# Performance work log

Measured on AMD Instinct MI355X. Metric: run time of the kernel, lower is better.

Reference implementation:

```python
import jax, jax.numpy as jnp
import numpy as np

N_MEMORY = 128
INPUT_LEN = 512
OUTPUT_LEN = 256
N_FRAMES = 65536


def setup_inputs() -> dict:
    key = jax.random.key(0)
    k1, k2, k3, k4, k5 = jax.random.split(key, 5)
    return {
        "inputs": jax.random.normal(k1, (INPUT_LEN, N_FRAMES), dtype=jnp.float32),
        "W1": jax.random.normal(k2, (2 * N_MEMORY, INPUT_LEN), dtype=jnp.float32) * 0.05,
        "B1": jax.random.normal(k3, (2 * N_MEMORY, 1), dtype=jnp.float32) * 0.05,
        "W2": jax.random.normal(k4, (OUTPUT_LEN, N_MEMORY), dtype=jnp.float32) * 0.05,
        "B2": jax.random.normal(k5, (OUTPUT_LEN, 1), dtype=jnp.float32) * 0.05,
    }


def reference(inputs, W1, B1, W2, B2):
    # h: (2M, T)
    h = jax.nn.sigmoid(jnp.matmul(W1, inputs) + B1)
    M = W1.shape[0] // 2
    left, right = h[:M], h[M:]          # each (M, T)
    prod = left * right                  # gate product, (M, T)

    # Linear recurrence: u_0 = 0; u_t = prod[:, t-1] * u_{t-1} + (1 - left[:, t-1])
    # Affine pairs for t = 1..T-1, time-major: (T-1, M)
    a = prod[:, :-1].T
    b = (1.0 - left[:, :-1]).T

    def combine(c1, c2):
        a1, b1 = c1
        a2, b2 = c2
        return a1 * a2, a2 * b1 + b2

    _, bb = jax.lax.associative_scan(combine, (a, b))
    # u_0 = 0 => u_t = bb_t; prepend the zero initial state as column 0
    z = jnp.concatenate([jnp.zeros((M, 1), dtype=inputs.dtype), bb.T], axis=1)  # (M, T)

    out = 1.0 - jax.nn.sigmoid(jnp.matmul(W2, z) + B2)  # (output_len, T)
    return out
```

## Files before the change

kernel.cpp:

```cpp
#include <hip/hip_runtime.h>

typedef unsigned short u16;
typedef short bf16x8 __attribute__((ext_vector_type(8)));
typedef float f32x4 __attribute__((ext_vector_type(4)));

#define NF 65536
#define GCH 512

__device__ __forceinline__ float sigm(float x){ return 1.0f/(1.0f+__expf(-x)); }

__device__ __forceinline__ u16 f2bf(float f){
  union { float f; unsigned u; } v; v.f = f;
  unsigned r = (v.u + 0x7fffu + ((v.u >> 16) & 1u)) >> 16;
  return (u16)r;
}

#define AS1(p) ((const __attribute__((address_space(1))) unsigned int*)(p))
#define AS3(p) ((__attribute__((address_space(3))) unsigned int*)(p))

__global__ __launch_bounds__(256) void k_prep(const float* __restrict__ W1, const float* __restrict__ W2,
                                              u16* __restrict__ W1f, u16* __restrict__ W2f){
  int idx = blockIdx.x*256 + threadIdx.x;
  {
    int j  = idx & 7;
    int L  = (idx >> 3) & 63;
    int ks = (idx >> 9) & 1;
    int rt = (idx >> 10) & 15;
    int ck = idx >> 14;
    int row = 16*rt + (L & 15);
    int k   = ck*64 + ks*32 + ((L >> 4) << 3) + j;
    W1f[idx] = f2bf(W1[row*512 + k]);
  }
  if (idx < 32768){
    int j  = idx & 7;
    int L  = (idx >> 3) & 63;
    int ks = (idx >> 9) & 3;
    int rt = idx >> 11;
    int row = 16*rt + (L & 15);
    int m   = ks*32 + ((L >> 4) << 3) + j;
    W2f[idx] = f2bf(W2[row*128 + m]);
  }
}

__global__ __launch_bounds__(256) void k_tr(const float* __restrict__ x, u16* __restrict__ xT){
  __shared__ float ls[64*65];
  const int tid = threadIdx.x;
  const int bt = blockIdx.x & 1023, bk = blockIdx.x >> 10;
  const int T0 = bt*64, K0 = bk*64;
  #pragma unroll
  for (int l=0;l<4;l++){
    int idx = tid + l*256;
    int kl = idx >> 4, c4 = idx & 15;
    float4 v = *(const float4*)(x + (size_t)(K0+kl)*NF + T0 + c4*4);
    float* d = ls + kl*65 + c4*4;
    d[0]=v.x; d[1]=v.y; d[2]=v.z; d[3]=v.w;
  }
  __syncthreads();
  #pragma unroll
  for (int l=0;l<2;l++){
    int p = tid + l*256;
    int t = p >> 3, kb = p & 7;
    unsigned u[8];
    #pragma unroll
    for (int m=0;m<8;m++) u[m] = f2bf(ls[(kb*8+m)*65 + t]);
    uint4 pk;
    pk.x = u[0] | (u[1]<<16); pk.y = u[2] | (u[3]<<16);
    pk.z = u[4] | (u[5]<<16); pk.w = u[6] | (u[7]<<16);
    *(uint4*)(xT + (size_t)(T0+t)*512 + K0 + kb*8) = pk;
  }
}

__global__ __launch_bounds__(256, 2) void k_gemm1(const u16* __restrict__ xT,
        const u16* __restrict__ W1f, const float* __restrict__ B1,
        float* __restrict__ Aa, float* __restrict__ Bb,
        float* __restrict__ Ac, float* __restrict__ Bc){
  __shared__ __align__(16) u16 ws[16384];
  __shared__ __align__(16) u16 xs[8192];
  const int tid = threadIdx.x;
  const int wv = tid >> 6, L = tid & 63;
  const int q = L >> 4, ln = L & 15;
  const int g = blockIdx.x;
  const int F0 = g * 128;
  const int rt0 = 2*wv;

  f32x4 acc[4][8];
  #pragma unroll
  for (int a=0;a<4;a++)
    #pragma unroll
    for (int c=0;c<8;c++) acc[a][c] = (f32x4){0.f,0.f,0.f,0.f};

  for (int ck=0; ck<8; ++ck){
    #pragma unroll
    for (int i=0;i<8;i++){
      int s = wv*8 + i;
      __builtin_amdgcn_global_load_lds(AS1(W1f + ck*16384 + s*512 + L*8), AS3(ws + s*512), 16, 0, 0);
    }
    #pragma unroll
    for (int i=0;i<4;i++){
      int s = wv*4 + i;
      int c = s >> 1, ks = s & 1;
      int t = F0 + c*16 + ln;
      int k = ck*64 + ks*32 + q*8;
      __builtin_amdgcn_global_load_lds(AS1(xT + (size_t)t*512 + k), AS3(xs + s*512), 16, 0, 0);
    }
    __syncthreads();
    #pragma unroll
    for (int ks=0; ks<2; ++ks){
      bf16x8 af[4];
      af[0] = ((const bf16x8*)ws)[( rt0   *2+ks)*64 + L];
      af[1] = ((const bf16x8*)ws)[((rt0+1)*2+ks)*64 + L];
      af[2] = ((const bf16x8*)ws)[((rt0+8)*2+ks)*64 + L];
      af[3] = ((const bf16x8*)ws)[((rt0+9)*2+ks)*64 + L];
      #pragma unroll
      for (int c=0;c<8;c++){
        bf16x8 bf = ((const bf16x8*)xs)[(c*2+ks)*64 + L];
        acc[0][c] = __builtin_amdgcn_mfma_f32_16x16x32_bf16(af[0], bf, acc[0][c], 0,0,0);
        acc[1][c] = __builtin_amdgcn_mfma_f32_16x16x32_bf16(af[1], bf, acc[1][c], 0,0,0);
        acc[2][c] = __builtin_amdgcn_mfma_f32_16x16x32_bf16(af[2], bf, acc[2][c], 0,0,0);
        acc[3][c] = __builtin_amdgcn_mfma_f32_16x16x32_bf16(af[3], bf, acc[3][c], 0,0,0);
      }
    }
    __syncthreads();
  }
  #pragma unroll
  for (int pr=0; pr<2; ++pr){
    int mb = 32*wv + 16*pr + 4*q;
    float bl[4], br[4];
    #pragma unroll
    for (int r=0;r<4;r++){ bl[r] = B1[mb+r]; br[r] = B1[mb+128+r]; }
    float RA[4], RB[4];
    #pragma unroll
    for (int c=0;c<8;c++){
      int t = F0 + 16*c + ln;
      f32x4 Lv = acc[pr][c], Rv = acc[pr+2][c];
      float a4[4], b4[4];
      #pragma unroll
      for (int r=0;r<4;r++){
        float le = sigm(Lv[r] + bl[r]);
        float ri = sigm(Rv[r] + br[r]);
        a4[r] = le*ri; b4[r] = 1.0f - le;
      }
      *(float4*)(Aa + (size_t)t*128 + mb) = make_float4(a4[0],a4[1],a4[2],a4[3]);
      *(float4*)(Bb + (size_t)t*128 + mb) = make_float4(b4[0],b4[1],b4[2],b4[3]);
      #pragma unroll
      for (int r=0;r<4;r++){
        float As = a4[r], Bs = b4[r];
        #pragma unroll
        for (int d=1; d<16; d<<=1){
          float Ap = __shfl_xor(As, d);
          float Bp = __shfl_xor(Bs, d);
          Bs = (ln & d) ? fmaf(As, Bp, Bs) : fmaf(Ap, Bs, Bp);
          As *= Ap;
        }
        if (c == 0){ RA[r] = As; RB[r] = Bs; }
        else       { RB[r] = fmaf(As, RB[r], Bs); RA[r] *= As; }
      }
    }
    if (ln == 0){
      #pragma unroll
      for (int r=0;r<4;r++){
        Ac[g*128 + mb + r] = RA[r];
        Bc[g*128 + mb + r] = RB[r];
      }
    }
  }
}

__global__ __launch_bounds__(1024) void k_scan(const float* __restrict__ Ac, const float* __restrict__ Bc,
                                               float* __restrict__ Pb){
  __shared__ float sA[8][128], sB[8][128];
  const int tid = threadIdx.x;
  const int m = tid & 127, s = tid >> 7;
  const int g0 = s*64;
  float A = 1.f, B = 0.f;
  #pragma unroll 16
  for (int i=0;i<64;i++){
    float a = Ac[(g0+i)*128 + m], b = Bc[(g0+i)*128 + m];
    B = fmaf(a, B, b);
    A *= a;
  }
  sA[s][m] = A; sB[s][m] = B;
  __syncthreads();
  float v = 0.f;
  for (int s2=0; s2<s; ++s2) v = fmaf(sA[s2][m], v, sB[s2][m]);
  #pragma unroll 16
  for (int i=0;i<64;i++){
    int g = g0+i;
    Pb[g*128+m] = v;
    v = fmaf(Ac[g*128+m], v, Bc[g*128+m]);
  }
}

__global__ __launch_bounds__(512, 2) void k_apply(const float* __restrict__ Aa, const float* __restrict__ Bb,
        const float* __restrict__ Pb, const u16* __restrict__ W2f, const float* __restrict__ B2,
        float* __restrict__ out){
  __shared__ __align__(16) u16 zf[16384];
  __shared__ float sA[4][128], sB[4][128];
  const int tid = threadIdx.x;
  const int g = blockIdx.x, T0 = g*128;

  {
    const int m = tid & 127, s4 = tid >> 7;
    const float* ap = Aa + (size_t)(T0 + s4*32)*128 + m;
    const float* bp = Bb + (size_t)(T0 + s4*32)*128 + m;
    float areg[32], breg[32];
    #pragma unroll
    for (int i=0;i<32;i++){ areg[i] = ap[(size_t)i*128]; breg[i] = bp[(size_t)i*128]; }
    float A = 1.f, Bv = 0.f;
    #pragma unroll
    for (int i=0;i<32;i++){ Bv = fmaf(areg[i], Bv, breg[i]); A *= areg[i]; }
    sA[s4][m] = A; sB[s4][m] = Bv;
    __syncthreads();
    float v = Pb[g*128 + m];
    for (int s2=0; s2<s4; ++s2) v = fmaf(sA[s2][m], v, sB[s2][m]);
    const int base_m = (m>>5)*512 + ((m>>3)&3)*128 + (m&7);
    #pragma unroll
    for (int i=0;i<32;i++){
      int t = s4*32 + i;
      zf[base_m + (t>>4)*2048 + (t&15)*8] = f2bf(v);
      v = fmaf(areg[i], v, breg[i]);
    }
  }
  __syncthreads();

  const int wv = tid >> 6, L = tid & 63;
  const int q = L >> 4, ln = L & 15;
  f32x4 acc[2][8];
  #pragma unroll
  for (int a=0;a<2;a++)
    #pragma unroll
    for (int c=0;c<8;c++) acc[a][c] = (f32x4){0.f,0.f,0.f,0.f};

  #pragma unroll
  for (int ks=0; ks<4; ++ks){
    bf16x8 af0 = ((const bf16x8*)W2f)[((2*wv  )*4+ks)*64 + L];
    bf16x8 af1 = ((const bf16x8*)W2f)[((2*wv+1)*4+ks)*64 + L];
    #pragma unroll
    for (int c=0;c<8;c++){
      bf16x8 bf = ((const bf16x8*)zf)[(c*4+ks)*64 + L];
      acc[0][c] = __builtin_amdgcn_mfma_f32_16x16x32_bf16(af0, bf, acc[0][c], 0,0,0);
      acc[1][c] = __builtin_amdgcn_mfma_f32_16x16x32_bf16(af1, bf, acc[1][c], 0,0,0);
    }
  }

  #pragma unroll
  for (int rs=0;rs<2;rs++){
    int rowb = (2*wv+rs)*16 + q*4;
    float b2[4];
    #pragma unroll
    for (int r=0;r<4;r++) b2[r] = B2[rowb+r];
    #pragma unroll
    for (int c=0;c<8;c++){
      int t = T0 + 16*c + ln;
      #pragma unroll
      for (int r=0;r<4;r++)
        out[(size_t)(rowb+r)*NF + t] = sigm(-(acc[rs][c][r] + b2[r]));
    }
  }
}

extern "C" void kernel_launch(void* const* d_in, const int* in_sizes, int n_in,
                              void* d_out, int out_size, void* d_ws, size_t ws_size,
                              hipStream_t stream) {
  const float* x  = (const float*)d_in[0];
  const float* W1 = (const float*)d_in[1];
  const float* B1 = (const float*)d_in[2];
  const float* W2 = (const float*)d_in[3];
  const float* B2 = (const float*)d_in[4];
  float* out = (float*)d_out;

  u16*   W1f = (u16*)d_ws;
  u16*   W2f = W1f + 131072;
  float* Aa  = (float*)d_ws + 81920;
  float* Bb  = Aa + (size_t)NF*128;
  float* Ac  = Bb + (size_t)NF*128;
  float* Bc  = Ac + (size_t)GCH*128;
  float* Pb  = Bc + (size_t)GCH*128;
  u16*   xT  = (u16*)d_out;

  k_prep <<<512, 256, 0, stream>>>(W1, W2, W1f, W2f);
  k_tr   <<<8192, 256, 0, stream>>>(x, xT);
  k_gemm1<<<512, 256, 0, stream>>>(xT, W1f, B1, Aa, Bb, Ac, Bc);
  k_scan <<<1, 1024, 0, stream>>>(Ac, Bc, Pb);
  k_apply<<<GCH, 512, 0, stream>>>(Aa, Bb, Pb, W2f, B2, out);
}
```

Measured before the change: 338.3 us.

## Fuse input transpose into GEMM1 and fold chunk scan into apply kernel

Removes the separate transpose kernel: GEMM1 now loads fp32 input tiles directly into LDS, converts them to bf16 and re-lays them out in shared memory before the MFMAs. W1 fragments are read straight from global memory into registers instead of being staged through LDS. The single-block carry-scan kernel is removed; each apply block recomputes its own prefix over preceding chunk summaries with four thread groups. This cuts two launches and a full bf16 round trip of the input through global memory, at the cost of in-kernel conversion work, redundant prefix computation per block, and a loop without the old trailing barrier.

```diff
diff --git a/kernel.cpp b/kernel.cpp
--- a/kernel.cpp
+++ b/kernel.cpp
@@ -42,46 +42,19 @@
   }
 }
 
-__global__ __launch_bounds__(256) void k_tr(const float* __restrict__ x, u16* __restrict__ xT){
-  __shared__ float ls[64*65];
-  const int tid = threadIdx.x;
-  const int bt = blockIdx.x & 1023, bk = blockIdx.x >> 10;
-  const int T0 = bt*64, K0 = bk*64;
-  #pragma unroll
-  for (int l=0;l<4;l++){
-    int idx = tid + l*256;
-    int kl = idx >> 4, c4 = idx & 15;
-    float4 v = *(const float4*)(x + (size_t)(K0+kl)*NF + T0 + c4*4);
-    float* d = ls + kl*65 + c4*4;
-    d[0]=v.x; d[1]=v.y; d[2]=v.z; d[3]=v.w;
-  }
-  __syncthreads();
-  #pragma unroll
-  for (int l=0;l<2;l++){
-    int p = tid + l*256;
-    int t = p >> 3, kb = p & 7;
-    unsigned u[8];
-    #pragma unroll
-    for (int m=0;m<8;m++) u[m] = f2bf(ls[(kb*8+m)*65 + t]);
-    uint4 pk;
-    pk.x = u[0] | (u[1]<<16); pk.y = u[2] | (u[3]<<16);
-    pk.z = u[4] | (u[5]<<16); pk.w = u[6] | (u[7]<<16);
-    *(uint4*)(xT + (size_t)(T0+t)*512 + K0 + kb*8) = pk;
-  }
-}
-
-__global__ __launch_bounds__(256, 2) void k_gemm1(const u16* __restrict__ xT,
+__global__ __launch_bounds__(256, 2) void k_gemm1(const float* __restrict__ x,
         const u16* __restrict__ W1f, const float* __restrict__ B1,
         float* __restrict__ Aa, float* __restrict__ Bb,
         float* __restrict__ Ac, float* __restrict__ Bc){
-  __shared__ __align__(16) u16 ws[16384];
-  __shared__ __align__(16) u16 xs[8192];
+  __shared__ __align__(16) float ls[8192];
+  __shared__ __align__(16) u16  xs[8192];
   const int tid = threadIdx.x;
   const int wv = tid >> 6, L = tid & 63;
   const int q = L >> 4, ln = L & 15;
   const int g = blockIdx.x;
   const int F0 = g * 128;
   const int rt0 = 2*wv;
+  const bf16x8* W1f8 = (const bf16x8*)W1f;
 
   f32x4 acc[4][8];
   #pragma unroll
@@ -92,36 +65,52 @@
   for (int ck=0; ck<8; ++ck){
     #pragma unroll
     for (int i=0;i<8;i++){
-      int s = wv*8 + i;
-      __builtin_amdgcn_global_load_lds(AS1(W1f + ck*16384 + s*512 + L*8), AS3(ws + s*512), 16, 0, 0);
-    }
+      int seg = wv*8 + i;
+      __builtin_amdgcn_global_load_lds(
+        AS1(x + (size_t)(ck*64 + seg*2 + (L>>5))*NF + F0 + (L&31)*4),
+        AS3(ls + seg*256), 16, 0, 0);
+    }
+    bf16x8 af[2][4];
+    #pragma unroll
+    for (int ks=0;ks<2;ks++){
+      af[ks][0] = W1f8[ck*2048 + ((rt0  )*2+ks)*64 + L];
+      af[ks][1] = W1f8[ck*2048 + ((rt0+1)*2+ks)*64 + L];
+      af[ks][2] = W1f8[ck*2048 + ((rt0+8)*2+ks)*64 + L];
+      af[ks][3] = W1f8[ck*2048 + ((rt0+9)*2+ks)*64 + L];
+    }
+    __syncthreads();
     #pragma unroll
     for (int i=0;i<4;i++){
-      int s = wv*4 + i;
-      int c = s >> 1, ks = s & 1;
-      int t = F0 + c*16 + ln;
-      int k = ck*64 + ks*32 + q*8;
-      __builtin_amdgcn_global_load_lds(AS1(xT + (size_t)t*512 + k), AS3(xs + s*512), 16, 0, 0);
+      int s    = tid + 256*i;
+      int lns  = s & 15;
+      int codd = (s >> 4) & 1;
+      int qs   = (s >> 5) & 3;
+      int chi  = (s >> 7) & 3;
+      int kss  = (s >> 9) & 1;
+      int cc   = chi*2 + codd;
+      const float* rp = ls + (kss*32 + qs*8)*128 + cc*16 + lns;
+      unsigned u[8];
+      #pragma unroll
+      for (int j=0;j<8;j++) u[j] = f2bf(rp[j*128]);
+      uint4 pk;
+      pk.x = u[0] | (u[1]<<16); pk.y = u[2] | (u[3]<<16);
+      pk.z = u[4] | (u[5]<<16); pk.w = u[6] | (u[7]<<16);
+      *(uint4*)(xs + ((cc*2+kss)*64 + qs*16 + lns)*8) = pk;
     }
     __syncthreads();
     #pragma unroll
     for (int ks=0; ks<2; ++ks){
-      bf16x8 af[4];
-      af[0] = ((const bf16x8*)ws)[( rt0   *2+ks)*64 + L];
-      af[1] = ((const bf16x8*)ws)[((rt0+1)*2+ks)*64 + L];
-      af[2] = ((const bf16x8*)ws)[((rt0+8)*2+ks)*64 + L];
-      af[3] = ((const bf16x8*)ws)[((rt0+9)*2+ks)*64 + L];
       #pragma unroll
       for (int c=0;c<8;c++){
         bf16x8 bf = ((const bf16x8*)xs)[(c*2+ks)*64 + L];
-        acc[0][c] = __builtin_amdgcn_mfma_f32_16x16x32_bf16(af[0], bf, acc[0][c], 0,0,0);
-        acc[1][c] = __builtin_amdgcn_mfma_f32_16x16x32_bf16(af[1], bf, acc[1][c], 0,0,0);
-        acc[2][c] = __builtin_amdgcn_mfma_f32_16x16x32_bf16(af[2], bf, acc[2][c], 0,0,0);
-        acc[3][c] = __builtin_amdgcn_mfma_f32_16x16x32_bf16(af[3], bf, acc[3][c], 0,0,0);
-      }
-    }
-    __syncthreads();
-  }
+        acc[0][c] = __builtin_amdgcn_mfma_f32_16x16x32_bf16(af[ks][0], bf, acc[0][c], 0,0,0);
+        acc[1][c] = __builtin_amdgcn_mfma_f32_16x16x32_bf16(af[ks][1], bf, acc[1][c], 0,0,0);
+        acc[2][c] = __builtin_amdgcn_mfma_f32_16x16x32_bf16(af[ks][2], bf, acc[2][c], 0,0,0);
+        acc[3][c] = __builtin_amdgcn_mfma_f32_16x16x32_bf16(af[ks][3], bf, acc[3][c], 0,0,0);
+      }
+    }
+  }
+  __syncthreads();
   #pragma unroll
   for (int pr=0; pr<2; ++pr){
     int mb = 32*wv + 16*pr + 4*q;
@@ -166,41 +155,36 @@
   }
 }
 
-__global__ __launch_bounds__(1024) void k_scan(const float* __restrict__ Ac, const float* __restrict__ Bc,
-                                               float* __restrict__ Pb){
-  __shared__ float sA[8][128], sB[8][128];
-  const int tid = threadIdx.x;
-  const int m = tid & 127, s = tid >> 7;
-  const int g0 = s*64;
-  float A = 1.f, B = 0.f;
-  #pragma unroll 16
-  for (int i=0;i<64;i++){
-    float a = Ac[(g0+i)*128 + m], b = Bc[(g0+i)*128 + m];
-    B = fmaf(a, B, b);
-    A *= a;
-  }
-  sA[s][m] = A; sB[s][m] = B;
-  __syncthreads();
-  float v = 0.f;
-  for (int s2=0; s2<s; ++s2) v = fmaf(sA[s2][m], v, sB[s2][m]);
-  #pragma unroll 16
-  for (int i=0;i<64;i++){
-    int g = g0+i;
-    Pb[g*128+m] = v;
-    v = fmaf(Ac[g*128+m], v, Bc[g*128+m]);
-  }
-}
-
 __global__ __launch_bounds__(512, 2) void k_apply(const float* __restrict__ Aa, const float* __restrict__ Bb,
-        const float* __restrict__ Pb, const u16* __restrict__ W2f, const float* __restrict__ B2,
+        const float* __restrict__ Ac, const float* __restrict__ Bc,
+        const u16* __restrict__ W2f, const float* __restrict__ B2,
         float* __restrict__ out){
   __shared__ __align__(16) u16 zf[16384];
   __shared__ float sA[4][128], sB[4][128];
   const int tid = threadIdx.x;
   const int g = blockIdx.x, T0 = g*128;
-
+  const int m = tid & 127, s4 = tid >> 7;
+
+  float vpref;
   {
-    const int m = tid & 127, s4 = tid >> 7;
+    int c0 = s4*128, c1 = c0 + 128; if (c1 > g) c1 = g;
+    float A = 1.f, B = 0.f;
+    #pragma unroll 4
+    for (int c = c0; c < c1; ++c){
+      float a = Ac[c*128 + m], b = Bc[c*128 + m];
+      B = fmaf(a, B, b);
+      A *= a;
+    }
+    sA[s4][m] = A; sB[s4][m] = B;
+    __syncthreads();
+    float v = 0.f;
+    #pragma unroll
+    for (int s2=0; s2<4; ++s2) v = fmaf(sA[s2][m], v, sB[s2][m]);
+    vpref = v;
+    __syncthreads();
+  }
+
+  {
     const float* ap = Aa + (size_t)(T0 + s4*32)*128 + m;
     const float* bp = Bb + (size_t)(T0 + s4*32)*128 + m;
     float areg[32], breg[32];
@@ -211,7 +195,7 @@
     for (int i=0;i<32;i++){ Bv = fmaf(areg[i], Bv, breg[i]); A *= areg[i]; }
     sA[s4][m] = A; sB[s4][m] = Bv;
     __syncthreads();
-    float v = Pb[g*128 + m];
+    float v = vpref;
     for (int s2=0; s2<s4; ++s2) v = fmaf(sA[s2][m], v, sB[s2][m]);
     const int base_m = (m>>5)*512 + ((m>>3)&3)*128 + (m&7);
     #pragma unroll
@@ -275,12 +259,8 @@
   float* Bb  = Aa + (size_t)NF*128;
   float* Ac  = Bb + (size_t)NF*128;
   float* Bc  = Ac + (size_t)GCH*128;
-  float* Pb  = Bc + (size_t)GCH*128;
-  u16*   xT  = (u16*)d_out;
 
   k_prep <<<512, 256, 0, stream>>>(W1, W2, W1f, W2f);
-  k_tr   <<<8192, 256, 0, stream>>>(x, xT);
-  k_gemm1<<<512, 256, 0, stream>>>(xT, W1f, B1, Aa, Bb, Ac, Bc);
-  k_scan <<<1, 1024, 0, stream>>>(Ac, Bc, Pb);
-  k_apply<<<GCH, 512, 0, stream>>>(Aa, Bb, Pb, W2f, B2, out);
-}
+  k_gemm1<<<512, 256, 0, stream>>>(x, W1f, B1, Aa, Bb, Ac, Bc);
+  k_apply<<<GCH, 512, 0, stream>>>(Aa, Bb, Ac, Bc, W2f, B2, out);
+}
```

Result: faster. 299.4 us (-11.5%).
